# Kernel optimization log

Hardware: AMD Instinct MI355X
Metric: run time of the kernel (lower is better)

The kernel has to match this reference:

```python
import jax, jax.numpy as jnp
import numpy as np

CHUNK = 64      # chunk_size
DIM = 128       # dim; memory state is a DIM x DIM fast-weight matrix (flattened)
BASE_LR = 0.005 # base inner-loop step size
META_LR = 0.01  # step size for the per-parameter learning-rate (optimizer) state


def setup_inputs():
    key = jax.random.key(0)
    k1, k2 = jax.random.split(key)
    B, L, D = 16, 8192, DIM
    X = jax.random.normal(k1, (B, L, D), jnp.float32)
    # init memory: small random D x D matrix, flattened (like LFLTM.init_params())
    init_mem = jax.random.normal(k2, (D * D,), jnp.float32) * 0.09
    # init optimizer state: per-parameter lr logits (sigmoid(0)=0.5)
    init_opt = jnp.zeros((D * D,), jnp.float32)
    return {"X": X, "init_mem": init_mem, "init_opt": init_opt}


def _forward(X, init_mem, init_opt):
    B, L, D = X.shape
    pad = (-L) % CHUNK
    Xp = jnp.pad(X, ((0, 0), (0, pad), (0, 0)))
    nC = Xp.shape[1] // CHUNK
    # [nC, B, CHUNK, D] so lax.scan iterates over chunks (the python loop in torch)
    Xc = Xp.reshape(B, nC, CHUNK, D).transpose(1, 0, 2, 3)

    def chunk_step(carry, x):
        mem, opt = carry                      # [B, D*D] each
        W = mem.reshape(B, D, D)
        # per-token gradient of 0.5*||W k - v||^2 with k = v = x, taken at the
        # chunk-start memory state (matches vmap(..., (0,0,None,None)) in torch)
        err = jnp.einsum('bij,bcj->bci', W, x) - x          # [B, C, D]
        g = jnp.einsum('bci,bcj->bcij', err, x).reshape(B, CHUNK, D * D)
        lr = jax.nn.sigmoid(opt)[:, None, :]                # [B, 1, D*D]
        mem_upd = BASE_LR * lr * g                          # memory update per token
        opt_upd = META_LR * (g * g) * lr * (1.0 - lr)       # lr-logit update per token
        cmu = jnp.cumsum(mem_upd, axis=1)                   # [B, C, D*D]
        cou = jnp.cumsum(opt_upd, axis=1)
        # memory path: state after each token's update (mem - cumsum)
        mem_path = (mem[:, None, :] - cmu).reshape(B, CHUNK, D, D)
        # retrieval: out_t = M_t @ q_t with q_t = x_t
        out = jnp.einsum('bcij,bcj->bci', mem_path, x)      # [B, C, D]
        new_carry = (mem - cmu[:, -1], opt - cou[:, -1])
        return new_carry, out

    mem0 = jnp.broadcast_to(init_mem, (B, D * D))
    opt0 = jnp.broadcast_to(init_opt, (B, D * D))
    _, outs = jax.lax.scan(chunk_step, (mem0, opt0), Xc)    # outs: [nC, B, C, D]
    outs = outs.transpose(1, 0, 2, 3).reshape(B, nC * CHUNK, D)
    return outs[:, :L]


def reference(X, init_mem, init_opt):
    return _forward(X, init_mem, init_opt)
```

## Files before the change

### kernel.cpp

```cpp
#include <hip/hip_runtime.h>
#include <math.h>

#define D 128
#define CHUNKSZ 64
#define NCHUNK 128
#define LSEQ 8192
#define BASE_LR 0.005f
#define META_LR 0.01f
#define XPAD 130

__global__ __launch_bounds__(512, 2) void lfltm_fwd(
    const float* __restrict__ X,
    const float* __restrict__ init_mem,
    const float* __restrict__ init_opt,
    float* __restrict__ out)
{
    __shared__ float xs[CHUNKSZ * XPAD];
    __shared__ float ms[8][D];
    __shared__ float es[8][CHUNKSZ];
    __shared__ float outs[CHUNKSZ][9];

    const int tid  = threadIdx.x;
    const int w    = tid >> 6;
    const int lane = tid & 63;

    const int bid  = blockIdx.x;
    const int xcd  = bid & 7;
    const int slot = bid >> 3;
    const int b    = xcd + 8 * (slot & 1);
    const int rg   = slot >> 1;
    const int i    = rg * 8 + w;

    const float* __restrict__ Xb = X + (size_t)b * (LSEQ * D);
    float* __restrict__ Ob       = out + (size_t)b * (LSEQ * D);

    float m0 = init_mem[i * D + 2 * lane];
    float m1 = init_mem[i * D + 2 * lane + 1];
    float o0 = init_opt[i * D + 2 * lane];
    float o1 = init_opt[i * D + 2 * lane + 1];
    float lr0 = 1.0f / (1.0f + expf(-o0));
    float lr1 = 1.0f / (1.0f + expf(-o1));

    float4 pf0, pf1, pf2, pf3;
    {
        const float4* src = (const float4*)Xb;
        pf0 = src[0 * 512 + tid];
        pf1 = src[1 * 512 + tid];
        pf2 = src[2 * 512 + tid];
        pf3 = src[3 * 512 + tid];
    }

    for (int ch = 0; ch < NCHUNK; ++ch) {
        {
            float4 v[4] = {pf0, pf1, pf2, pf3};
            #pragma unroll
            for (int r = 0; r < 4; ++r) {
                int f = (r * 512 + tid) * 4;
                int c = f >> 7;
                int j = f & (D - 1);
                float* dst = &xs[c * XPAD + j];
                *(float2*)(dst)     = make_float2(v[r].x, v[r].y);
                *(float2*)(dst + 2) = make_float2(v[r].z, v[r].w);
            }
        }
        *(float2*)&ms[w][2 * lane] = make_float2(m0, m1);

        __syncthreads();

        {
            int chn = (ch + 1 < NCHUNK) ? ch + 1 : ch;
            const float4* src = (const float4*)(Xb + (size_t)chn * (CHUNKSZ * D));
            pf0 = src[0 * 512 + tid];
            pf1 = src[1 * 512 + tid];
            pf2 = src[2 * 512 + tid];
            pf3 = src[3 * 512 + tid];
        }

        const float* xrow = &xs[lane * XPAD];
        float acc0 = 0.f, acc1 = 0.f, acc2 = 0.f, acc3 = 0.f;
        #pragma unroll
        for (int jq = 0; jq < D / 4; ++jq) {
            float4 m4  = *(const float4*)&ms[w][jq * 4];
            float2 xa  = *(const float2*)&xrow[jq * 4];
            float2 xb2 = *(const float2*)&xrow[jq * 4 + 2];
            acc0 = fmaf(m4.x, xa.x,  acc0);
            acc1 = fmaf(m4.y, xa.y,  acc1);
            acc2 = fmaf(m4.z, xb2.x, acc2);
            acc3 = fmaf(m4.w, xb2.y, acc3);
        }
        float dotv = (acc0 + acc1) + (acc2 + acc3);
        float e = dotv - xrow[i];
        es[w][lane] = e;
        asm volatile("s_waitcnt lgkmcnt(0)" ::: "memory");

        float S0 = 0.f, S1 = 0.f, Q0 = 0.f, Q1 = 0.f;
        float parr[CHUNKSZ];
        #pragma unroll
        for (int cq = 0; cq < CHUNKSZ / 4; ++cq) {
            float4 e4 = *(const float4*)&es[w][cq * 4];
            #pragma unroll
            for (int u = 0; u < 4; ++u) {
                const int c = cq * 4 + u;
                float ec = (u == 0) ? e4.x : (u == 1) ? e4.y : (u == 2) ? e4.z : e4.w;
                float2 x2 = *(const float2*)&xs[c * XPAD + 2 * lane];
                float ex0 = ec * x2.x;
                float ex1 = ec * x2.y;
                S0 += ex0;
                S1 += ex1;
                float pc = (lr0 * x2.x) * S0;
                pc = fmaf(lr1 * x2.y, S1, pc);
                Q0 = fmaf(ex0, ex0, Q0);
                Q1 = fmaf(ex1, ex1, Q1);
                parr[c] = pc;
            }
        }

        #pragma unroll
        for (int o = 32; o >= 1; o >>= 1) {
            const bool hi = (lane & o) != 0;
            #pragma unroll
            for (int t = 0; t < o; ++t) {
                float send = hi ? parr[t] : parr[t + o];
                float recv = __shfl_xor(send, o, 64);
                parr[t] = (hi ? parr[t + o] : parr[t]) + recv;
            }
        }
        outs[lane][w] = dotv - BASE_LR * parr[0];

        m0 = fmaf(-BASE_LR * lr0, S0, m0);
        m1 = fmaf(-BASE_LR * lr1, S1, m1);
        o0 = fmaf(-META_LR * lr0 * (1.f - lr0), Q0, o0);
        o1 = fmaf(-META_LR * lr1 * (1.f - lr1), Q1, o1);
        lr0 = 1.0f / (1.0f + expf(-o0));
        lr1 = 1.0f / (1.0f + expf(-o1));

        __syncthreads();

        {
            int c  = tid >> 3;
            int ww = tid & 7;
            Ob[(size_t)(ch * CHUNKSZ + c) * D + rg * 8 + ww] = outs[c][ww];
        }
    }
}

extern "C" void kernel_launch(void* const* d_in, const int* in_sizes, int n_in,
                              void* d_out, int out_size, void* d_ws, size_t ws_size,
                              hipStream_t stream) {
    const float* X  = (const float*)d_in[0];
    const float* im = (const float*)d_in[1];
    const float* io = (const float*)d_in[2];
    float* O        = (float*)d_out;
    hipLaunchKernelGGL(lfltm_fwd, dim3(256), dim3(512), 0, stream, X, im, io, O);
}
```

Baseline: 662.2 us.

## Double-buffer chunks via direct global-to-LDS loads and compute dot products with butterfly reduction

Replaces the register prefetch and LDS store with asynchronous global_load_lds into a double-buffered LDS chunk, and moves the output write-back one iteration later. The W·x dot product is now computed from each lane's own two columns and reduced with a permlane/DPP/swizzle butterfly instead of reading the shared memory row. Packed FP32 math (v_pk_mul/v_pk_fma) and fast __expf replace scalar ops, which removes a barrier and the ms staging. The cost is higher register pressure from holding 64 x-pairs per lane, with launch bounds reduced to one block per CU, plus an extra uncoalesced global read per lane for x[c][i].

```diff
diff --git a/kernel.cpp b/kernel.cpp
--- a/kernel.cpp
+++ b/kernel.cpp
@@ -2,146 +2,162 @@
 #include <math.h>
 
 #define D 128
-#define CHUNKSZ 64
+#define CHK 64
 #define NCHUNK 128
 #define LSEQ 8192
-#define BASE_LR 0.005f
-#define META_LR 0.01f
-#define XPAD 130
+#define B_LR 0.005f
+#define M_LR 0.01f
 
-__global__ __launch_bounds__(512, 2) void lfltm_fwd(
+typedef float f2 __attribute__((ext_vector_type(2)));
+
+__device__ __forceinline__ f2 pk_mul(f2 a, f2 b){ f2 d; asm("v_pk_mul_f32 %0, %1, %2" : "=v"(d) : "v"(a), "v"(b)); return d; }
+__device__ __forceinline__ f2 pk_fma(f2 a, f2 b, f2 c){ f2 d; asm("v_pk_fma_f32 %0, %1, %2, %3" : "=v"(d) : "v"(a), "v"(b), "v"(c)); return d; }
+
+template<int C>
+__device__ __forceinline__ float dppx(float x){
+  return __int_as_float(__builtin_amdgcn_update_dpp(0, __float_as_int(x), C, 0xF, 0xF, true));
+}
+__device__ __forceinline__ void pl32swap(float &a, float &b){ asm("v_permlane32_swap_b32 %0, %1" : "+v"(a), "+v"(b)); }
+__device__ __forceinline__ void pl16swap(float &a, float &b){ asm("v_permlane16_swap_b32 %0, %1" : "+v"(a), "+v"(b)); }
+
+__device__ __forceinline__ float butterfly64(float* a, int lane){
+  #pragma unroll
+  for (int t = 0; t < 32; ++t){ float u=a[t], w=a[t+32]; pl32swap(u,w); a[t]=u+w; }
+  #pragma unroll
+  for (int t = 0; t < 16; ++t){ float u=a[t], w=a[t+16]; pl16swap(u,w); a[t]=u+w; }
+  const bool h8 = (lane & 8) != 0, h4 = (lane & 4) != 0, h2 = (lane & 2) != 0, h1 = (lane & 1) != 0;
+  #pragma unroll
+  for (int t = 0; t < 8; ++t){
+    float send = h8 ? a[t] : a[t+8];
+    float keep = h8 ? a[t+8] : a[t];
+    a[t] = keep + dppx<0x128>(send);
+  }
+  #pragma unroll
+  for (int t = 0; t < 4; ++t){
+    float send = h4 ? a[t] : a[t+4];
+    float keep = h4 ? a[t+4] : a[t];
+    a[t] = keep + __int_as_float(__builtin_amdgcn_ds_swizzle(__float_as_int(send), 0x101F));
+  }
+  #pragma unroll
+  for (int t = 0; t < 2; ++t){
+    float send = h2 ? a[t] : a[t+2];
+    float keep = h2 ? a[t+2] : a[t];
+    a[t] = keep + dppx<0x4E>(send);
+  }
+  float send = h1 ? a[0] : a[1];
+  float keep = h1 ? a[1] : a[0];
+  return keep + dppx<0xB1>(send);
+}
+
+__device__ __forceinline__ void gl_lds16(const float* g, float* l){
+  __builtin_amdgcn_global_load_lds((const __attribute__((address_space(1))) float*)g,
+                                   (__attribute__((address_space(3))) float*)l, 16, 0, 0);
+}
+
+__global__ __launch_bounds__(512, 1) void lfltm_fwd(
     const float* __restrict__ X,
     const float* __restrict__ init_mem,
     const float* __restrict__ init_opt,
     float* __restrict__ out)
 {
-    __shared__ float xs[CHUNKSZ * XPAD];
-    __shared__ float ms[8][D];
-    __shared__ float es[8][CHUNKSZ];
-    __shared__ float outs[CHUNKSZ][9];
+  __shared__ float xs[2][CHK * D];
+  __shared__ float es[8][CHK];
+  __shared__ float outs[2][CHK * 9];
 
-    const int tid  = threadIdx.x;
-    const int w    = tid >> 6;
-    const int lane = tid & 63;
+  const int tid  = threadIdx.x;
+  const int w    = tid >> 6;
+  const int lane = tid & 63;
 
-    const int bid  = blockIdx.x;
-    const int xcd  = bid & 7;
-    const int slot = bid >> 3;
-    const int b    = xcd + 8 * (slot & 1);
-    const int rg   = slot >> 1;
-    const int i    = rg * 8 + w;
+  const int bid  = blockIdx.x;
+  const int xcd  = bid & 7;
+  const int slot = bid >> 3;
+  const int b    = xcd + 8 * (slot & 1);
+  const int rg   = slot >> 1;
+  const int i    = rg * 8 + w;
 
-    const float* __restrict__ Xb = X + (size_t)b * (LSEQ * D);
-    float* __restrict__ Ob       = out + (size_t)b * (LSEQ * D);
+  const float* __restrict__ Xb = X + (size_t)b * (LSEQ * D);
+  float* __restrict__ Ob       = out + (size_t)b * (LSEQ * D);
 
-    float m0 = init_mem[i * D + 2 * lane];
-    float m1 = init_mem[i * D + 2 * lane + 1];
-    float o0 = init_opt[i * D + 2 * lane];
-    float o1 = init_opt[i * D + 2 * lane + 1];
-    float lr0 = 1.0f / (1.0f + expf(-o0));
-    float lr1 = 1.0f / (1.0f + expf(-o1));
+  float m0 = init_mem[i * D + 2*lane];
+  float m1 = init_mem[i * D + 2*lane + 1];
+  float o0 = init_opt[i * D + 2*lane];
+  float o1 = init_opt[i * D + 2*lane + 1];
+  const float u0 = (2*lane     == i) ? 1.0f : 0.0f;
+  const float u1 = (2*lane + 1 == i) ? 1.0f : 0.0f;
 
-    float4 pf0, pf1, pf2, pf3;
-    {
-        const float4* src = (const float4*)Xb;
-        pf0 = src[0 * 512 + tid];
-        pf1 = src[1 * 512 + tid];
-        pf2 = src[2 * 512 + tid];
-        pf3 = src[3 * 512 + tid];
+  #pragma unroll
+  for (int r = 0; r < 4; ++r)
+    gl_lds16(Xb + (r*512 + tid)*4, &xs[0][(r*512 + tid)*4]);
+  __syncthreads();
+
+  for (int ch = 0; ch < NCHUNK; ++ch) {
+    const int cur = ch & 1;
+
+    if (ch > 0) {
+      const int c = tid >> 3, ww = tid & 7;
+      Ob[(size_t)((ch-1)*CHK + c)*D + rg*8 + ww] = outs[cur ^ 1][c*9 + ww];
     }
 
-    for (int ch = 0; ch < NCHUNK; ++ch) {
-        {
-            float4 v[4] = {pf0, pf1, pf2, pf3};
-            #pragma unroll
-            for (int r = 0; r < 4; ++r) {
-                int f = (r * 512 + tid) * 4;
-                int c = f >> 7;
-                int j = f & (D - 1);
-                float* dst = &xs[c * XPAD + j];
-                *(float2*)(dst)     = make_float2(v[r].x, v[r].y);
-                *(float2*)(dst + 2) = make_float2(v[r].z, v[r].w);
-            }
-        }
-        *(float2*)&ms[w][2 * lane] = make_float2(m0, m1);
+    {
+      int chn = ch + 1; if (chn >= NCHUNK) chn = NCHUNK - 1;
+      const float* gb = Xb + (size_t)chn * (CHK * D);
+      #pragma unroll
+      for (int r = 0; r < 4; ++r)
+        gl_lds16(gb + (r*512 + tid)*4, &xs[cur ^ 1][(r*512 + tid)*4]);
+    }
 
-        __syncthreads();
+    const float xci = Xb[(size_t)(ch*CHK + lane)*D + i];
 
-        {
-            int chn = (ch + 1 < NCHUNK) ? ch + 1 : ch;
-            const float4* src = (const float4*)(Xb + (size_t)chn * (CHUNKSZ * D));
-            pf0 = src[0 * 512 + tid];
-            pf1 = src[1 * 512 + tid];
-            pf2 = src[2 * 512 + tid];
-            pf3 = src[3 * 512 + tid];
-        }
+    const float lr0 = 1.0f / (1.0f + __expf(-o0));
+    const float lr1 = 1.0f / (1.0f + __expf(-o1));
+    f2 lr2; lr2.x = lr0; lr2.y = lr1;
+    f2 mp;  mp.x = m0 - u0; mp.y = m1 - u1;
 
-        const float* xrow = &xs[lane * XPAD];
-        float acc0 = 0.f, acc1 = 0.f, acc2 = 0.f, acc3 = 0.f;
-        #pragma unroll
-        for (int jq = 0; jq < D / 4; ++jq) {
-            float4 m4  = *(const float4*)&ms[w][jq * 4];
-            float2 xa  = *(const float2*)&xrow[jq * 4];
-            float2 xb2 = *(const float2*)&xrow[jq * 4 + 2];
-            acc0 = fmaf(m4.x, xa.x,  acc0);
-            acc1 = fmaf(m4.y, xa.y,  acc1);
-            acc2 = fmaf(m4.z, xb2.x, acc2);
-            acc3 = fmaf(m4.w, xb2.y, acc3);
-        }
-        float dotv = (acc0 + acc1) + (acc2 + acc3);
-        float e = dotv - xrow[i];
-        es[w][lane] = e;
-        asm volatile("s_waitcnt lgkmcnt(0)" ::: "memory");
+    f2 xr[CHK];
+    float arr[CHK];
+    const float* xb = &xs[cur][2*lane];
+    #pragma unroll
+    for (int c = 0; c < CHK; ++c){
+      xr[c] = *(const f2*)(xb + c*D);
+      f2 t = pk_mul(mp, xr[c]);
+      arr[c] = t.x + t.y;
+    }
+    const float e_own = butterfly64(arr, lane);
+    es[w][lane] = e_own;
 
-        float S0 = 0.f, S1 = 0.f, Q0 = 0.f, Q1 = 0.f;
-        float parr[CHUNKSZ];
-        #pragma unroll
-        for (int cq = 0; cq < CHUNKSZ / 4; ++cq) {
-            float4 e4 = *(const float4*)&es[w][cq * 4];
-            #pragma unroll
-            for (int u = 0; u < 4; ++u) {
-                const int c = cq * 4 + u;
-                float ec = (u == 0) ? e4.x : (u == 1) ? e4.y : (u == 2) ? e4.z : e4.w;
-                float2 x2 = *(const float2*)&xs[c * XPAD + 2 * lane];
-                float ex0 = ec * x2.x;
-                float ex1 = ec * x2.y;
-                S0 += ex0;
-                S1 += ex1;
-                float pc = (lr0 * x2.x) * S0;
-                pc = fmaf(lr1 * x2.y, S1, pc);
-                Q0 = fmaf(ex0, ex0, Q0);
-                Q1 = fmaf(ex1, ex1, Q1);
-                parr[c] = pc;
-            }
-        }
+    f2 Sp; Sp.x = 0.f; Sp.y = 0.f;
+    f2 Q2; Q2.x = 0.f; Q2.y = 0.f;
+    #pragma unroll
+    for (int cg = 0; cg < CHK/4; ++cg){
+      float4 e4 = *(const float4*)&es[w][cg*4];
+      #pragma unroll
+      for (int u = 0; u < 4; ++u){
+        const int c = cg*4 + u;
+        const float ec = (u==0)?e4.x:(u==1)?e4.y:(u==2)?e4.z:e4.w;
+        f2 e2; e2.x = ec; e2.y = ec;
+        f2 ex  = pk_mul(e2, xr[c]);
+        Sp     = pk_fma(lr2, ex, Sp);
+        f2 pc2 = pk_mul(xr[c], Sp);
+        Q2     = pk_fma(ex, ex, Q2);
+        arr[c] = pc2.x + pc2.y;
+      }
+    }
+    const float p = butterfly64(arr, lane);
 
-        #pragma unroll
-        for (int o = 32; o >= 1; o >>= 1) {
-            const bool hi = (lane & o) != 0;
-            #pragma unroll
-            for (int t = 0; t < o; ++t) {
-                float send = hi ? parr[t] : parr[t + o];
-                float recv = __shfl_xor(send, o, 64);
-                parr[t] = (hi ? parr[t + o] : parr[t]) + recv;
-            }
-        }
-        outs[lane][w] = dotv - BASE_LR * parr[0];
+    outs[cur][lane*9 + w] = e_own + xci - B_LR * p;
 
-        m0 = fmaf(-BASE_LR * lr0, S0, m0);
-        m1 = fmaf(-BASE_LR * lr1, S1, m1);
-        o0 = fmaf(-META_LR * lr0 * (1.f - lr0), Q0, o0);
-        o1 = fmaf(-META_LR * lr1 * (1.f - lr1), Q1, o1);
-        lr0 = 1.0f / (1.0f + expf(-o0));
-        lr1 = 1.0f / (1.0f + expf(-o1));
+    m0 = fmaf(-B_LR, Sp.x, m0);
+    m1 = fmaf(-B_LR, Sp.y, m1);
+    o0 = fmaf(-M_LR * lr0 * (1.f - lr0), Q2.x, o0);
+    o1 = fmaf(-M_LR * lr1 * (1.f - lr1), Q2.y, o1);
 
-        __syncthreads();
+    __syncthreads();
+  }
 
-        {
-            int c  = tid >> 3;
-            int ww = tid & 7;
-            Ob[(size_t)(ch * CHUNKSZ + c) * D + rg * 8 + ww] = outs[c][ww];
-        }
-    }
+  {
+    const int c = tid >> 3, ww = tid & 7;
+    Ob[(size_t)((NCHUNK-1)*CHK + c)*D + rg*8 + ww] = outs[(NCHUNK-1)&1][c*9 + ww];
+  }
 }
 
 extern "C" void kernel_launch(void* const* d_in, const int* in_sizes, int n_in,
```

New measurement: 578.6 us. 1.14x faster.
